# Performance work log

Hardware: AMD Instinct MI355X
Metric: run time of the kernel (lower is better)

The kernel has to match this reference:

```python
import jax, jax.numpy as jnp
import numpy as np

D_MODEL = 1024
H = 16
D_K = D_MODEL // H
NEG = -1e9


def setup_inputs() -> dict:
    key = jax.random.key(0)
    ks = jax.random.split(key, 13)
    B, S = 4, 2048
    q = jax.random.normal(ks[0], (B, S, D_MODEL), dtype=jnp.float32)
    k = jax.random.normal(ks[1], (B, S, D_MODEL), dtype=jnp.float32)
    v = jax.random.normal(ks[2], (B, S, D_MODEL), dtype=jnp.float32)
    mask = jax.random.randint(ks[3], (B, 1, S, S), 0, 2, dtype=jnp.int32)
    s = 1.0 / np.sqrt(D_MODEL)
    wq = jax.random.uniform(ks[4], (D_MODEL, D_MODEL), jnp.float32, -s, s)
    bq = jax.random.uniform(ks[5], (D_MODEL,), jnp.float32, -s, s)
    wk = jax.random.uniform(ks[6], (D_MODEL, D_MODEL), jnp.float32, -s, s)
    bk = jax.random.uniform(ks[7], (D_MODEL,), jnp.float32, -s, s)
    wv = jax.random.uniform(ks[8], (D_MODEL, D_MODEL), jnp.float32, -s, s)
    bv = jax.random.uniform(ks[9], (D_MODEL,), jnp.float32, -s, s)
    wo = jax.random.uniform(ks[10], (D_MODEL, D_MODEL), jnp.float32, -s, s)
    bo = jax.random.uniform(ks[11], (D_MODEL,), jnp.float32, -s, s)
    return {"q": q, "k": k, "v": v, "mask": mask,
            "wq": wq, "bq": bq, "wk": wk, "bk": bk,
            "wv": wv, "bv": bv, "wo": wo, "bo": bo}


def reference(q, k, v, mask, wq, bq, wk, bk, wv, bv, wo, bo):
    B, S, _ = q.shape
    # projections (torch Linear: x @ W.T + b)
    query = q @ wq.T + bq
    key_ = k @ wk.T + bk
    value = v @ wv.T + bv
    # [B, S, H, D_K] -> [B, H, S, D_K]
    query = query.reshape(B, S, H, D_K).transpose(0, 2, 1, 3)
    key_ = key_.reshape(B, S, H, D_K).transpose(0, 2, 1, 3)
    value = value.reshape(B, S, H, D_K).transpose(0, 2, 1, 3)
    scores = jnp.einsum('bhqd,bhkd->bhqk', query, key_) / jnp.sqrt(jnp.float32(D_K))
    scores = jnp.where(mask == 0, jnp.float32(NEG), scores)
    attn = jax.nn.softmax(scores, axis=-1)  # dropout p=0 -> identity
    x = jnp.einsum('bhqk,bhkd->bhqd', attn, value)
    x = x.transpose(0, 2, 1, 3).reshape(B, S, D_MODEL)
    return x @ wo.T + bo
```

## Files before the change

### kernel.cpp

```cpp
#include <hip/hip_runtime.h>
#include <stdint.h>
#include <stddef.h>


typedef unsigned short ushort_t;
typedef unsigned long long u64;
typedef __attribute__((ext_vector_type(8))) short short8;
typedef __attribute__((ext_vector_type(4))) float floatx4;
typedef __attribute__((ext_vector_type(4))) unsigned short ushort4v;
typedef __attribute__((ext_vector_type(4))) unsigned int uint4v;

#define QSCALE (0.125f * 1.4426950408889634f)

__device__ __forceinline__ ushort_t f2bf(float f) {
    union { float ff; unsigned int i; } v; v.ff = f;
    unsigned int u = v.i;
    return (ushort_t)((u + 0x7fffu + ((u >> 16) & 1u)) >> 16);
}
__device__ __forceinline__ unsigned int pk2(float a, float b) {
    unsigned int r;
    asm("v_cvt_pk_bf16_f32 %0, %1, %2" : "=v"(r) : "v"(a), "v"(b));
    return r;
}
__device__ __forceinline__ float fexp2(float x) {
#if __has_builtin(__builtin_amdgcn_exp2f)
    return __builtin_amdgcn_exp2f(x);
#else
    return exp2f(x);
#endif
}
__device__ __forceinline__ void g2l16(const void* g, void* l) {
    __builtin_amdgcn_global_load_lds(
        (const __attribute__((address_space(1))) void*)(uintptr_t)g,
        (__attribute__((address_space(3))) void*)(uint32_t)(uintptr_t)l,
        16, 0, 0);
}
__device__ __forceinline__ void cvt_store(ushort_t* d0, ushort_t* d1,
        float4 a, float4 b, float4 c, float4 d) {
    uint4v c0, c1;
    c0.x = pk2(a.x, a.y); c0.y = pk2(a.z, a.w);
    c0.z = pk2(b.x, b.y); c0.w = pk2(b.z, b.w);
    c1.x = pk2(c.x, c.y); c1.y = pk2(c.z, c.w);
    c1.z = pk2(d.x, d.y); c1.w = pk2(d.z, d.w);
    *(uint4v*)d0 = c0;
    *(uint4v*)d1 = c1;
}

__global__ __launch_bounds__(256) void prep(
    const float* __restrict__ wq, const float* __restrict__ wk,
    const float* __restrict__ wv, const float* __restrict__ wo,
    const int* __restrict__ mask,
    ushort_t* __restrict__ Wb, u64* __restrict__ mbits)
{
    const int bx = blockIdx.x, tid = threadIdx.x;
    if (bx < 2048) {
        const int seg = bx >> 9;
        const float* src = (seg == 0) ? wq : (seg == 1) ? wk
                         : (seg == 2) ? wv : wo;
        ushort_t* dst = Wb + (size_t)seg * 1024 * 1024;
        const int idx = (bx & 511) * 256 + tid;
        const float4 f0 = ((const float4*)src)[idx * 2];
        const float4 f1 = ((const float4*)src)[idx * 2 + 1];
        uint4v c;
        c.x = pk2(f0.x, f0.y); c.y = pk2(f0.z, f0.w);
        c.z = pk2(f1.x, f1.y); c.w = pk2(f1.z, f1.w);
        ((uint4v*)dst)[idx] = c;
    } else {
        const int b3 = bx - 2048;
        const int base = b3 * 4096;
#pragma unroll
        for (int it = 0; it < 16; ++it) {
            const int gid = base + it * 256 + tid;
            const u64 bits = __ballot(mask[gid] != 0);
            if ((tid & 63) == 0) mbits[gid >> 6] = bits;
        }
    }
}

__device__ __forceinline__ void gemm_epilogue(
    floatx4 (&acc)[4][4], const float* __restrict__ bias,
    void* __restrict__ Cout, float scale, int mode,
    int bm, int bn, int wm, int wn, int quad, int l16)
{
#pragma unroll
    for (int ni = 0; ni < 4; ni++) {
        const int n = bn + wn * 64 + ni * 16 + l16;
        const float bv_ = bias[n];
#pragma unroll
        for (int mi = 0; mi < 4; mi++) {
            const int mbase = bm + wm * 64 + mi * 16 + quad * 4;
            if (mode == 2) {
                const int b_ = mbase >> 11, s0 = mbase & 2047;
                const int h = n >> 6, d = n & 63;
                ushort4v pk_;
#pragma unroll
                for (int r = 0; r < 4; r++)
                    pk_[r] = f2bf((acc[mi][ni][r] + bv_) * scale);
                *(ushort4v*)&((ushort_t*)Cout)[
                    (((size_t)(b_ * 16 + h)) * 64 + d) * 2048 + s0] = pk_;
            } else {
#pragma unroll
                for (int r = 0; r < 4; r++) {
                    const int m = mbase + r;
                    const float of = (acc[mi][ni][r] + bv_) * scale;
                    const int b_ = m >> 11, s = m & 2047;
                    const int h = n >> 6, d = n & 63;
                    ((ushort_t*)Cout)[(((size_t)(b_ * 16 + h)) * 2048 + s) * 64 + d]
                        = f2bf(of);
                }
            }
        }
    }
}

__device__ __forceinline__ void gemm_core_f32(
    const float* __restrict__ Ain, const ushort_t* __restrict__ W,
    const float* __restrict__ bias, void* __restrict__ Cout,
    float scale, int mode)
{
    constexpr int K = 1024;
    __shared__ alignas(16) ushort_t As[2][128 * 32];
    __shared__ alignas(16) ushort_t Bs[2][128 * 32];

    const int tid  = threadIdx.x;
    const int lane = tid & 63;
    const int w    = tid >> 6;
    const int quad = lane >> 4;
    const int l16  = lane & 15;
    const int wm = w >> 1, wn = w & 1;
    const int bm = blockIdx.x * 128, bn = blockIdx.y * 128;

    const int wrow = tid >> 2;
    const int wcs  = ((tid & 3) ^ ((tid >> 3) & 3)) * 8;
    const ushort_t* Wst0 = W + (size_t)(bn + wrow) * K + wcs;
    const ushort_t* Wst1 = W + (size_t)(bn + wrow + 64) * K + wcs;

    const int arow = tid >> 1, ahalf = tid & 1;
    const float* Af = Ain + (size_t)(bm + arow) * K + ahalf * 16;
    const int fa  = (tid >> 2) & 3;
    const int ac0 = ((2 * ahalf + 0) ^ fa) * 8;
    const int ac1 = ((2 * ahalf + 1) ^ fa) * 8;

    const int ksw = (quad ^ ((l16 >> 1) & 3)) * 8;
    int asoff[4], bsoff[4];
#pragma unroll
    for (int i = 0; i < 4; i++) {
        asoff[i] = (wm * 64 + i * 16 + l16) * 32 + ksw;
        bsoff[i] = (wn * 64 + i * 16 + l16) * 32 + ksw;
    }

    floatx4 acc[4][4] = {};

    {
        const float4* ap = (const float4*)Af;
        const float4 f0 = ap[0], f1 = ap[1], f2 = ap[2], f3 = ap[3];
        g2l16(Wst0, &Bs[0][tid * 8]);
        g2l16(Wst1, &Bs[0][(tid + 256) * 8]);
        cvt_store(&As[0][arow * 32 + ac0], &As[0][arow * 32 + ac1],
                  f0, f1, f2, f3);
    }
    __syncthreads();

    int cur = 0;
    for (int kt = 0; kt < K; kt += 32) {
        const int nxt = kt + 32;
        float4 f0, f1, f2, f3;
        if (nxt < K) {
            const float4* ap = (const float4*)(Af + nxt);
            f0 = ap[0]; f1 = ap[1]; f2 = ap[2]; f3 = ap[3];
            g2l16(Wst0 + nxt, &Bs[cur ^ 1][tid * 8]);
            g2l16(Wst1 + nxt, &Bs[cur ^ 1][(tid + 256) * 8]);
        }

        short8 af[4], bf[4];
#pragma unroll
        for (int i = 0; i < 4; i++) af[i] = *(const short8*)&As[cur][asoff[i]];
#pragma unroll
        for (int i = 0; i < 4; i++) bf[i] = *(const short8*)&Bs[cur][bsoff[i]];
#pragma unroll
        for (int mi = 0; mi < 4; mi++)
#pragma unroll
            for (int ni = 0; ni < 4; ni++)
                acc[mi][ni] = __builtin_amdgcn_mfma_f32_16x16x32_bf16(
                    af[mi], bf[ni], acc[mi][ni], 0, 0, 0);

        if (nxt < K)
            cvt_store(&As[cur ^ 1][arow * 32 + ac0],
                      &As[cur ^ 1][arow * 32 + ac1], f0, f1, f2, f3);
        __syncthreads();
        cur ^= 1;
    }

    gemm_epilogue(acc, bias, Cout, scale, mode, bm, bn, wm, wn, quad, l16);
}

__global__ __launch_bounds__(256, 3) void gemm_qkv(
    const float* __restrict__ q, const float* __restrict__ k,
    const float* __restrict__ v, const ushort_t* __restrict__ Wb,
    const float* __restrict__ bq, const float* __restrict__ bk,
    const float* __restrict__ bv,
    ushort_t* __restrict__ Qp, ushort_t* __restrict__ Kp,
    ushort_t* __restrict__ Vtp)
{
    const int z = blockIdx.z;
    const float* A = (z == 0) ? q : (z == 1) ? k : v;
    const ushort_t* W = Wb + (size_t)z * 1024 * 1024;
    const float* bi = (z == 0) ? bq : (z == 1) ? bk : bv;
    void* C = (z == 0) ? (void*)Qp : (z == 1) ? (void*)Kp : (void*)Vtp;
    const float sc = (z == 0) ? QSCALE : 1.0f;
    const int mode = (z == 2) ? 2 : 1;
    gemm_core_f32(A, W, bi, C, sc, mode);
}

__global__ __launch_bounds__(256, 4) void gemm_out(
    const ushort_t* __restrict__ Ain, const ushort_t* __restrict__ W,
    const float* __restrict__ bias, float* __restrict__ out)
{
    constexpr int K = 1024, N = 1024;
    __shared__ alignas(16) ushort_t As[4][64 * 32];
    __shared__ alignas(16) ushort_t Bs[2][128 * 32];

    const int tid  = threadIdx.x;
    const int lane = tid & 63;
    const int w    = tid >> 6;
    const int quad = lane >> 4;
    const int l16  = lane & 15;
    const int wm = w >> 1, wn = w & 1;
    const int bm = blockIdx.x * 64, bn = blockIdx.y * 128;

    const int srow = tid >> 2;
    const int scs  = ((tid & 3) ^ ((tid >> 3) & 3)) * 8;
    const ushort_t* Ast  = Ain + (size_t)(bm + srow) * K + scs;
    const ushort_t* Wst0 = W + (size_t)(bn + srow) * K + scs;
    const ushort_t* Wst1 = W + (size_t)(bn + srow + 64) * K + scs;

    const int ksw = (quad ^ ((l16 >> 1) & 3)) * 8;
    int asoff[2], bsoff[4];
#pragma unroll
    for (int i = 0; i < 2; i++)
        asoff[i] = (wm * 32 + i * 16 + l16) * 32 + ksw;
#pragma unroll
    for (int i = 0; i < 4; i++)
        bsoff[i] = (wn * 64 + i * 16 + l16) * 32 + ksw;

    floatx4 acc[2][4] = {};

    g2l16(Wst0,      &Bs[0][tid * 8]);
    g2l16(Wst1,      &Bs[0][(tid + 256) * 8]);
    __builtin_amdgcn_sched_barrier(0);
    g2l16(Ast,       &As[0][tid * 8]);
    g2l16(Ast + 32,  &As[1][tid * 8]);
    g2l16(Ast + 64,  &As[2][tid * 8]);

#define OITER(AS, WS, NW, NA, KW, KA, DO_W, DO_A, TOPW) do {                  \
    asm volatile("s_waitcnt " TOPW);                                          \
    asm volatile("s_waitcnt lgkmcnt(0)");                                     \
    __builtin_amdgcn_sched_barrier(0);                                        \
    __builtin_amdgcn_s_barrier();                                             \
    __builtin_amdgcn_sched_barrier(0);                                        \
    if (DO_W) {                                                               \
        g2l16(Wst0 + (KW), &Bs[NW][tid * 8]);                                 \
        g2l16(Wst1 + (KW), &Bs[NW][(tid + 256) * 8]);                         \
    }                                                                         \
    __builtin_amdgcn_sched_barrier(0);                                        \
    if (DO_A) g2l16(Ast + (KA), &As[NA][tid * 8]);                            \
    __builtin_amdgcn_sched_barrier(0);                                        \
    {                                                                         \
        short8 af[2], bf[4];                                                  \
        _Pragma("unroll")                                                     \
        for (int i = 0; i < 2; i++) af[i] = *(const short8*)&As[AS][asoff[i]];\
        _Pragma("unroll")                                                     \
        for (int i = 0; i < 4; i++) bf[i] = *(const short8*)&Bs[WS][bsoff[i]];\
        _Pragma("unroll")                                                     \
        for (int mi = 0; mi < 2; mi++)                                        \
        _Pragma("unroll")                                                     \
        for (int ni = 0; ni < 4; ni++)                                        \
            acc[mi][ni] = __builtin_amdgcn_mfma_f32_16x16x32_bf16(            \
                af[mi], bf[ni], acc[mi][ni], 0, 0, 0);                        \
    }                                                                         \
} while (0)

    OITER(0, 0, 1, 3,  32,  96, true, true, "vmcnt(2)");
    OITER(1, 1, 0, 0,  64, 128, true, true, "vmcnt(1)");
    OITER(2, 0, 1, 1,  96, 160, true, true, "vmcnt(1)");
    OITER(3, 1, 0, 2, 128, 192, true, true, "vmcnt(1)");
    for (int j = 1; j < 7; ++j) {
        const int kb = j * 128;
        OITER(0, 0, 1, 3, kb + 32,  kb + 96,  true, true, "vmcnt(1)");
        OITER(1, 1, 0, 0, kb + 64,  kb + 128, true, true, "vmcnt(1)");
        OITER(2, 0, 1, 1, kb + 96,  kb + 160, true, true, "vmcnt(1)");
        OITER(3, 1, 0, 2, kb + 128, kb + 192, true, true, "vmcnt(1)");
    }
    OITER(0, 0, 1, 3, 928, 992, true,  true,  "vmcnt(1)");
    OITER(1, 1, 0, 0, 960, 0,   true,  false, "vmcnt(1)");
    OITER(2, 0, 1, 0, 992, 0,   true,  false, "vmcnt(0)");
    OITER(3, 1, 0, 0, 0,   0,   false, false, "vmcnt(0)");
#undef OITER

#pragma unroll
    for (int ni = 0; ni < 4; ni++) {
        const int n = bn + wn * 64 + ni * 16 + l16;
        const float bv_ = bias[n];
#pragma unroll
        for (int mi = 0; mi < 2; mi++) {
            const int mbase = bm + wm * 32 + mi * 16 + quad * 4;
#pragma unroll
            for (int r = 0; r < 4; r++)
                out[(size_t)(mbase + r) * N + n] = acc[mi][ni][r] + bv_;
        }
    }
}

__global__ __launch_bounds__(256, 4) void attn(
    const ushort_t* __restrict__ Q,
    const ushort_t* __restrict__ Kk,
    const ushort_t* __restrict__ Vt,
    const u64* __restrict__ mb,
    ushort_t* __restrict__ X)
{
    constexpr int S = 2048;
    __shared__ alignas(16) ushort_t Ks[2][64 * 64];
    __shared__ alignas(16) ushort_t Vs[2][64 * 64];
    __shared__ alignas(16) ushort_t Ps[4][16 * 64];

    const int tid  = threadIdx.x;
    const int lane = tid & 63;
    const int w    = tid >> 6;
    const int quad = lane >> 4;
    const int l16  = lane & 15;
    const int bh = blockIdx.x;
    const int b  = bh >> 4, h = bh & 15;
    const int qbase = blockIdx.y * 64 + w * 16;
    const int qlane = qbase + l16;

    const int r0 = tid >> 3,         cs0 = ((tid & 7) ^ (r0 & 7)) * 8;
    const int r1 = (tid + 256) >> 3, cs1 = ((tid & 7) ^ (r1 & 7)) * 8;

    const ushort_t* Kst0 = &Kk[((size_t)bh * S + r0) * 64 + cs0];
    const ushort_t* Kst1 = &Kk[((size_t)bh * S + r1) * 64 + cs1];
    const ushort_t* Vst0 = &Vt[((size_t)bh * 64 + r0) * S + cs0];
    const ushort_t* Vst1 = &Vt[((size_t)bh * 64 + r1) * S + cs1];

    const int swz = l16 & 7;
    int kvoff[2][4], pfoff[2], pwoff[4];
#pragma unroll
    for (int ks = 0; ks < 2; ks++) {
        pfoff[ks] = l16 * 64 + (((ks * 4 + quad) ^ swz) * 8);
#pragma unroll
        for (int ni = 0; ni < 4; ni++)
            kvoff[ks][ni] = (ni * 16 + l16) * 64 + (((ks * 4 + quad) ^ swz) * 8);
    }
#pragma unroll
    for (int ni = 0; ni < 4; ni++)
        pwoff[ni] = l16 * 64 + (((ni * 2 + (quad >> 1)) ^ swz) * 8) + (quad & 1) * 4;
    ushort_t* Psw = &Ps[w][0];

    short8 qf[2];
#pragma unroll
    for (int ks = 0; ks < 2; ks++)
        qf[ks] = *(const short8*)&Q[((size_t)bh * S + qlane) * 64 + ks * 32 + quad * 8];

    short8 onesv;
#pragma unroll
    for (int i = 0; i < 8; i++) onesv[i] = (short)0x3F80;

    const u64* mrow = mb + ((size_t)b * S + qlane) * 32;

    floatx4 o[4] = {};
    floatx4 lf = {};

    g2l16(Kst0, &Ks[0][tid * 8]);
    g2l16(Kst1, &Ks[0][(tid + 256) * 8]);
    g2l16(Vst0, &Vs[0][tid * 8]);
    g2l16(Vst1, &Vs[0][(tid + 256) * 8]);
    __syncthreads();

    u64 mw = mrow[0];
    int cur = 0;
    for (int kt = 0; kt < 32; kt++) {
        u64 mw_nxt = 0;
        if (kt < 31) {
            mw_nxt = mrow[kt + 1];
            g2l16(Kst0 + (kt + 1) * 4096, &Ks[cur ^ 1][tid * 8]);
            g2l16(Kst1 + (kt + 1) * 4096, &Ks[cur ^ 1][(tid + 256) * 8]);
            g2l16(Vst0 + (kt + 1) * 64,   &Vs[cur ^ 1][tid * 8]);
            g2l16(Vst1 + (kt + 1) * 64,   &Vs[cur ^ 1][(tid + 256) * 8]);
        }
        const ushort_t* Ksc = &Ks[cur][0];
        const ushort_t* Vsc = &Vs[cur][0];

        floatx4 s[4] = {};
        __builtin_amdgcn_s_setprio(1);
#pragma unroll
        for (int ks = 0; ks < 2; ks++)
#pragma unroll
            for (int ni = 0; ni < 4; ni++)
                s[ni] = __builtin_amdgcn_mfma_f32_16x16x32_bf16(
                    *(const short8*)&Ksc[kvoff[ks][ni]], qf[ks], s[ni], 0, 0, 0);
        __builtin_amdgcn_s_setprio(0);

#pragma unroll
        for (int ni = 0; ni < 4; ni++) {
            const unsigned int t = (unsigned int)(mw >> (ni * 16 + quad * 4));
#pragma unroll
            for (int r = 0; r < 4; r++)
                s[ni][r] = (t & (1u << r)) ? fexp2(s[ni][r]) : 0.f;
        }

#pragma unroll
        for (int ni = 0; ni < 4; ni++) {
            const unsigned int lo = pk2(s[ni][0], s[ni][1]);
            const unsigned int hi = pk2(s[ni][2], s[ni][3]);
            const unsigned long long dv = ((unsigned long long)hi << 32) | lo;
            *(unsigned long long*)&Psw[pwoff[ni]] = dv;
        }

        __builtin_amdgcn_s_setprio(1);
#pragma unroll
        for (int ks = 0; ks < 2; ks++) {
            const short8 pf = *(const short8*)&Psw[pfoff[ks]];
            lf = __builtin_amdgcn_mfma_f32_16x16x32_bf16(onesv, pf, lf, 0, 0, 0);
#pragma unroll
            for (int ni = 0; ni < 4; ni++)
                o[ni] = __builtin_amdgcn_mfma_f32_16x16x32_bf16(
                    *(const short8*)&Vsc[kvoff[ks][ni]], pf, o[ni], 0, 0, 0);
        }
        __builtin_amdgcn_s_setprio(0);
        __syncthreads();
        mw = mw_nxt;
        cur ^= 1;
    }

    const float inv = 1.0f / lf[0];
#pragma unroll
    for (int ni = 0; ni < 4; ni++) {
        ushort4v pk_;
#pragma unroll
        for (int r = 0; r < 4; r++) pk_[r] = f2bf(o[ni][r] * inv);
        *(ushort4v*)&X[((size_t)b * S + qlane) * 1024 + h * 64 + ni * 16 + quad * 4] = pk_;
    }
}

extern "C" void kernel_launch(void* const* d_in, const int* in_sizes, int n_in,
                              void* d_out, int out_size, void* d_ws, size_t ws_size,
                              hipStream_t stream) {
    const float* q    = (const float*)d_in[0];
    const float* k    = (const float*)d_in[1];
    const float* v    = (const float*)d_in[2];
    const int*   mask = (const int*)d_in[3];
    const float* wq   = (const float*)d_in[4];
    const float* bq   = (const float*)d_in[5];
    const float* wk   = (const float*)d_in[6];
    const float* bk   = (const float*)d_in[7];
    const float* wv   = (const float*)d_in[8];
    const float* bv   = (const float*)d_in[9];
    const float* wo   = (const float*)d_in[10];
    const float* bo   = (const float*)d_in[11];

    const size_t MB = 1024 * 1024;
    uint8_t* ws = (uint8_t*)d_ws;
    ushort_t* Wb   = (ushort_t*)(ws);
    u64*      mbits= (u64*)(ws + 8 * MB);
    ushort_t* Qp   = (ushort_t*)(ws + 10 * MB);
    ushort_t* Kp   = (ushort_t*)(ws + 26 * MB);
    ushort_t* Vtp  = (ushort_t*)(ws + 42 * MB);
    ushort_t* Xp   = (ushort_t*)(ws + 58 * MB);

    dim3 blk(256);

    prep<<<dim3(6144), blk, 0, stream>>>(wq, wk, wv, wo, mask, Wb, mbits);

    gemm_qkv<<<dim3(64, 8, 3), blk, 0, stream>>>(q, k, v, Wb, bq, bk, bv,
                                                 Qp, Kp, Vtp);

    attn<<<dim3(64, 32), blk, 0, stream>>>(Qp, Kp, Vtp, mbits, Xp);

    gemm_out<<<dim3(128, 8), blk, 0, stream>>>(Xp, Wb + 3 * MB, bo, (float*)d_out);
}
```

Baseline: 428.0 us.

## Enlarge QKV GEMM tile to 256 rows and route fp32 attention output to generic GEMM

The QKV projection becomes a 512-thread kernel with a 256x128 tile, so each weight tile loaded into shared memory serves twice as many rows. The attention kernel now writes fp32 output instead of bf16, and the output projection drops its hand-scheduled bf16 pipeline in favour of the generic fp32-input GEMM core that converts on load. This is meant to improve weight reuse in the projection, but it doubles the attention output traffic and gives up the tuned software pipeline in the output GEMM.

```diff
diff --git a/kernel.cpp b/kernel.cpp
--- a/kernel.cpp
+++ b/kernel.cpp
@@ -77,11 +77,92 @@
     }
 }
 
-__device__ __forceinline__ void gemm_epilogue(
-    floatx4 (&acc)[4][4], const float* __restrict__ bias,
-    void* __restrict__ Cout, float scale, int mode,
-    int bm, int bn, int wm, int wn, int quad, int l16)
+__global__ __launch_bounds__(512, 3) void gemm_qkv(
+    const float* __restrict__ q, const float* __restrict__ k,
+    const float* __restrict__ v, const ushort_t* __restrict__ Wb,
+    const float* __restrict__ bq, const float* __restrict__ bk,
+    const float* __restrict__ bv,
+    ushort_t* __restrict__ Qp, ushort_t* __restrict__ Kp,
+    ushort_t* __restrict__ Vtp)
 {
+    constexpr int K = 1024;
+    __shared__ alignas(16) ushort_t As[2][256 * 32];
+    __shared__ alignas(16) ushort_t Bs[2][128 * 32];
+
+    const int z = blockIdx.z;
+    const float* Ain = (z == 0) ? q : (z == 1) ? k : v;
+    const ushort_t* W = Wb + (size_t)z * 1024 * 1024;
+    const float* bias = (z == 0) ? bq : (z == 1) ? bk : bv;
+    void* Cout = (z == 0) ? (void*)Qp : (z == 1) ? (void*)Kp : (void*)Vtp;
+    const float scale = (z == 0) ? QSCALE : 1.0f;
+    const int mode = (z == 2) ? 2 : 1;
+
+    const int tid  = threadIdx.x;
+    const int lane = tid & 63;
+    const int w    = tid >> 6;
+    const int quad = lane >> 4;
+    const int l16  = lane & 15;
+    const int wm = w >> 1, wn = w & 1;
+    const int bm = blockIdx.x * 256, bn = blockIdx.y * 128;
+
+    const int wrow = tid >> 2;
+    const int wcs  = ((tid & 3) ^ ((tid >> 3) & 3)) * 8;
+    const ushort_t* Wst = W + (size_t)(bn + wrow) * K + wcs;
+
+    const int arow = tid >> 1, ahalf = tid & 1;
+    const float* Af = Ain + (size_t)(bm + arow) * K + ahalf * 16;
+    const int fa  = (tid >> 2) & 3;
+    const int ac0 = ((2 * ahalf + 0) ^ fa) * 8;
+    const int ac1 = ((2 * ahalf + 1) ^ fa) * 8;
+
+    const int ksw = (quad ^ ((l16 >> 1) & 3)) * 8;
+    int asoff[4], bsoff[4];
+#pragma unroll
+    for (int i = 0; i < 4; i++) {
+        asoff[i] = (wm * 64 + i * 16 + l16) * 32 + ksw;
+        bsoff[i] = (wn * 64 + i * 16 + l16) * 32 + ksw;
+    }
+
+    floatx4 acc[4][4] = {};
+
+    {
+        const float4* ap = (const float4*)Af;
+        const float4 f0 = ap[0], f1 = ap[1], f2 = ap[2], f3 = ap[3];
+        g2l16(Wst, &Bs[0][tid * 8]);
+        cvt_store(&As[0][arow * 32 + ac0], &As[0][arow * 32 + ac1],
+                  f0, f1, f2, f3);
+    }
+    __syncthreads();
+
+    int cur = 0;
+    for (int kt = 0; kt < K; kt += 32) {
+        const int nxt = kt + 32;
+        float4 f0, f1, f2, f3;
+        if (nxt < K) {
+            const float4* ap = (const float4*)(Af + nxt);
+            f0 = ap[0]; f1 = ap[1]; f2 = ap[2]; f3 = ap[3];
+            g2l16(Wst + nxt, &Bs[cur ^ 1][tid * 8]);
+        }
+
+        short8 af[4], bf[4];
+#pragma unroll
+        for (int i = 0; i < 4; i++) af[i] = *(const short8*)&As[cur][asoff[i]];
+#pragma unroll
+        for (int i = 0; i < 4; i++) bf[i] = *(const short8*)&Bs[cur][bsoff[i]];
+#pragma unroll
+        for (int mi = 0; mi < 4; mi++)
+#pragma unroll
+            for (int ni = 0; ni < 4; ni++)
+                acc[mi][ni] = __builtin_amdgcn_mfma_f32_16x16x32_bf16(
+                    af[mi], bf[ni], acc[mi][ni], 0, 0, 0);
+
+        if (nxt < K)
+            cvt_store(&As[cur ^ 1][arow * 32 + ac0],
+                      &As[cur ^ 1][arow * 32 + ac1], f0, f1, f2, f3);
+        __syncthreads();
+        cur ^= 1;
+    }
+
 #pragma unroll
     for (int ni = 0; ni < 4; ni++) {
         const int n = bn + wn * 64 + ni * 16 + l16;
@@ -113,12 +194,11 @@
     }
 }
 
-__device__ __forceinline__ void gemm_core_f32(
+__global__ __launch_bounds__(256, 3) void gemm_out(
     const float* __restrict__ Ain, const ushort_t* __restrict__ W,
-    const float* __restrict__ bias, void* __restrict__ Cout,
-    float scale, int mode)
+    const float* __restrict__ bias, float* __restrict__ out)
 {
-    constexpr int K = 1024;
+    constexpr int K = 1024, N = 1024;
     __shared__ alignas(16) ushort_t As[2][128 * 32];
     __shared__ alignas(16) ushort_t Bs[2][128 * 32];
 
@@ -191,119 +271,13 @@
         cur ^= 1;
     }
 
-    gemm_epilogue(acc, bias, Cout, scale, mode, bm, bn, wm, wn, quad, l16);
-}
-
-__global__ __launch_bounds__(256, 3) void gemm_qkv(
-    const float* __restrict__ q, const float* __restrict__ k,
-    const float* __restrict__ v, const ushort_t* __restrict__ Wb,
-    const float* __restrict__ bq, const float* __restrict__ bk,
-    const float* __restrict__ bv,
-    ushort_t* __restrict__ Qp, ushort_t* __restrict__ Kp,
-    ushort_t* __restrict__ Vtp)
-{
-    const int z = blockIdx.z;
-    const float* A = (z == 0) ? q : (z == 1) ? k : v;
-    const ushort_t* W = Wb + (size_t)z * 1024 * 1024;
-    const float* bi = (z == 0) ? bq : (z == 1) ? bk : bv;
-    void* C = (z == 0) ? (void*)Qp : (z == 1) ? (void*)Kp : (void*)Vtp;
-    const float sc = (z == 0) ? QSCALE : 1.0f;
-    const int mode = (z == 2) ? 2 : 1;
-    gemm_core_f32(A, W, bi, C, sc, mode);
-}
-
-__global__ __launch_bounds__(256, 4) void gemm_out(
-    const ushort_t* __restrict__ Ain, const ushort_t* __restrict__ W,
-    const float* __restrict__ bias, float* __restrict__ out)
-{
-    constexpr int K = 1024, N = 1024;
-    __shared__ alignas(16) ushort_t As[4][64 * 32];
-    __shared__ alignas(16) ushort_t Bs[2][128 * 32];
-
-    const int tid  = threadIdx.x;
-    const int lane = tid & 63;
-    const int w    = tid >> 6;
-    const int quad = lane >> 4;
-    const int l16  = lane & 15;
-    const int wm = w >> 1, wn = w & 1;
-    const int bm = blockIdx.x * 64, bn = blockIdx.y * 128;
-
-    const int srow = tid >> 2;
-    const int scs  = ((tid & 3) ^ ((tid >> 3) & 3)) * 8;
-    const ushort_t* Ast  = Ain + (size_t)(bm + srow) * K + scs;
-    const ushort_t* Wst0 = W + (size_t)(bn + srow) * K + scs;
-    const ushort_t* Wst1 = W + (size_t)(bn + srow + 64) * K + scs;
-
-    const int ksw = (quad ^ ((l16 >> 1) & 3)) * 8;
-    int asoff[2], bsoff[4];
-#pragma unroll
-    for (int i = 0; i < 2; i++)
-        asoff[i] = (wm * 32 + i * 16 + l16) * 32 + ksw;
-#pragma unroll
-    for (int i = 0; i < 4; i++)
-        bsoff[i] = (wn * 64 + i * 16 + l16) * 32 + ksw;
-
-    floatx4 acc[2][4] = {};
-
-    g2l16(Wst0,      &Bs[0][tid * 8]);
-    g2l16(Wst1,      &Bs[0][(tid + 256) * 8]);
-    __builtin_amdgcn_sched_barrier(0);
-    g2l16(Ast,       &As[0][tid * 8]);
-    g2l16(Ast + 32,  &As[1][tid * 8]);
-    g2l16(Ast + 64,  &As[2][tid * 8]);
-
-#define OITER(AS, WS, NW, NA, KW, KA, DO_W, DO_A, TOPW) do {                  \
-    asm volatile("s_waitcnt " TOPW);                                          \
-    asm volatile("s_waitcnt lgkmcnt(0)");                                     \
-    __builtin_amdgcn_sched_barrier(0);                                        \
-    __builtin_amdgcn_s_barrier();                                             \
-    __builtin_amdgcn_sched_barrier(0);                                        \
-    if (DO_W) {                                                               \
-        g2l16(Wst0 + (KW), &Bs[NW][tid * 8]);                                 \
-        g2l16(Wst1 + (KW), &Bs[NW][(tid + 256) * 8]);                         \
-    }                                                                         \
-    __builtin_amdgcn_sched_barrier(0);                                        \
-    if (DO_A) g2l16(Ast + (KA), &As[NA][tid * 8]);                            \
-    __builtin_amdgcn_sched_barrier(0);                                        \
-    {                                                                         \
-        short8 af[2], bf[4];                                                  \
-        _Pragma("unroll")                                                     \
-        for (int i = 0; i < 2; i++) af[i] = *(const short8*)&As[AS][asoff[i]];\
-        _Pragma("unroll")                                                     \
-        for (int i = 0; i < 4; i++) bf[i] = *(const short8*)&Bs[WS][bsoff[i]];\
-        _Pragma("unroll")                                                     \
-        for (int mi = 0; mi < 2; mi++)                                        \
-        _Pragma("unroll")                                                     \
-        for (int ni = 0; ni < 4; ni++)                                        \
-            acc[mi][ni] = __builtin_amdgcn_mfma_f32_16x16x32_bf16(            \
-                af[mi], bf[ni], acc[mi][ni], 0, 0, 0);                        \
-    }                                                                         \
-} while (0)
-
-    OITER(0, 0, 1, 3,  32,  96, true, true, "vmcnt(2)");
-    OITER(1, 1, 0, 0,  64, 128, true, true, "vmcnt(1)");
-    OITER(2, 0, 1, 1,  96, 160, true, true, "vmcnt(1)");
-    OITER(3, 1, 0, 2, 128, 192, true, true, "vmcnt(1)");
-    for (int j = 1; j < 7; ++j) {
-        const int kb = j * 128;
-        OITER(0, 0, 1, 3, kb + 32,  kb + 96,  true, true, "vmcnt(1)");
-        OITER(1, 1, 0, 0, kb + 64,  kb + 128, true, true, "vmcnt(1)");
-        OITER(2, 0, 1, 1, kb + 96,  kb + 160, true, true, "vmcnt(1)");
-        OITER(3, 1, 0, 2, kb + 128, kb + 192, true, true, "vmcnt(1)");
-    }
-    OITER(0, 0, 1, 3, 928, 992, true,  true,  "vmcnt(1)");
-    OITER(1, 1, 0, 0, 960, 0,   true,  false, "vmcnt(1)");
-    OITER(2, 0, 1, 0, 992, 0,   true,  false, "vmcnt(0)");
-    OITER(3, 1, 0, 0, 0,   0,   false, false, "vmcnt(0)");
-#undef OITER
-
 #pragma unroll
     for (int ni = 0; ni < 4; ni++) {
         const int n = bn + wn * 64 + ni * 16 + l16;
         const float bv_ = bias[n];
 #pragma unroll
-        for (int mi = 0; mi < 2; mi++) {
-            const int mbase = bm + wm * 32 + mi * 16 + quad * 4;
+        for (int mi = 0; mi < 4; mi++) {
+            const int mbase = bm + wm * 64 + mi * 16 + quad * 4;
 #pragma unroll
             for (int r = 0; r < 4; r++)
                 out[(size_t)(mbase + r) * N + n] = acc[mi][ni][r] + bv_;
@@ -316,7 +290,7 @@
     const ushort_t* __restrict__ Kk,
     const ushort_t* __restrict__ Vt,
     const u64* __restrict__ mb,
-    ushort_t* __restrict__ X)
+    float* __restrict__ X)
 {
     constexpr int S = 2048;
     __shared__ alignas(16) ushort_t Ks[2][64 * 64];
@@ -434,10 +408,10 @@
     const float inv = 1.0f / lf[0];
 #pragma unroll
     for (int ni = 0; ni < 4; ni++) {
-        ushort4v pk_;
-#pragma unroll
-        for (int r = 0; r < 4; r++) pk_[r] = f2bf(o[ni][r] * inv);
-        *(ushort4v*)&X[((size_t)b * S + qlane) * 1024 + h * 64 + ni * 16 + quad * 4] = pk_;
+        float4 st;
+        st.x = o[ni][0] * inv; st.y = o[ni][1] * inv;
+        st.z = o[ni][2] * inv; st.w = o[ni][3] * inv;
+        *(float4*)&X[((size_t)b * S + qlane) * 1024 + h * 64 + ni * 16 + quad * 4] = st;
     }
 }
 
@@ -464,16 +438,16 @@
     ushort_t* Qp   = (ushort_t*)(ws + 10 * MB);
     ushort_t* Kp   = (ushort_t*)(ws + 26 * MB);
     ushort_t* Vtp  = (ushort_t*)(ws + 42 * MB);
-    ushort_t* Xp   = (ushort_t*)(ws + 58 * MB);
+    float*    Xp   = (float*)(ws + 58 * MB);
 
     dim3 blk(256);
 
     prep<<<dim3(6144), blk, 0, stream>>>(wq, wk, wv, wo, mask, Wb, mbits);
 
-    gemm_qkv<<<dim3(64, 8, 3), blk, 0, stream>>>(q, k, v, Wb, bq, bk, bv,
-                                                 Qp, Kp, Vtp);
+    gemm_qkv<<<dim3(32, 8, 3), dim3(512), 0, stream>>>(q, k, v, Wb, bq, bk, bv,
+                                                       Qp, Kp, Vtp);
 
     attn<<<dim3(64, 32), blk, 0, stream>>>(Qp, Kp, Vtp, mbits, Xp);
 
-    gemm_out<<<dim3(128, 8), blk, 0, stream>>>(Xp, Wb + 3 * MB, bo, (float*)d_out);
-}
+    gemm_out<<<dim3(64, 8), blk, 0, stream>>>(Xp, Wb + 3 * MB, bo, (float*)d_out);
+}
```

Result: slower. 452.6 us (+5.7%).
